# Optimization experiments

Hardware: AMD Instinct MI355X
Metric: run time of the kernel (lower is better)

## Reference

```python
import jax, jax.numpy as jnp
import numpy as np


def setup_inputs() -> dict:
    key = jax.random.key(0)
    ks = jax.random.split(key, 8)
    B, L, D, N, K = 4, 4096, 1024, 64, 4
    return {
        "x": jax.random.normal(ks[0], (B, L, D), dtype=jnp.float32),
        "conv_w": jax.random.normal(ks[1], (K, 1, D), dtype=jnp.float32) * 0.1,
        "conv_b": jnp.zeros((D,), dtype=jnp.float32),
        "Wp": jax.random.normal(ks[2], (D, 2 * N), dtype=jnp.float32) * (1.0 / np.sqrt(D)),
        "bp": jnp.zeros((2 * N,), dtype=jnp.float32),
        "Ws": jax.random.normal(ks[3], (D, N), dtype=jnp.float32) * (1.0 / np.sqrt(D)),
        "bs": jnp.zeros((N,), dtype=jnp.float32),
        "A_log": jax.random.normal(ks[4], (N,), dtype=jnp.float32) * 0.02,
        "dt_log": jax.random.normal(ks[5], (N,), dtype=jnp.float32) * 0.02,
        "Wo": jax.random.normal(ks[6], (N, D), dtype=jnp.float32) * (1.0 / np.sqrt(N)),
        "bo": jnp.zeros((D,), dtype=jnp.float32),
    }


def reference(x, conv_w, conv_b, Wp, bp, Ws, bs, A_log, dt_log, Wo, bo):
    B, L, D = x.shape
    K = conv_w.shape[0]
    N = Ws.shape[1]

    # causal depthwise conv: left-pad by K-1, sum K shifted slices (K is tiny)
    x_pad = jnp.pad(x, ((0, 0), (K - 1, 0), (0, 0)))
    conv = conv_b + sum(x_pad[:, k:k + L, :] * conv_w[k, 0] for k in range(K))

    proj = conv @ Wp + bp                     # [B, L, 2N]
    B_t = jax.nn.softplus(proj[..., :N])      # [B, L, N]
    C_t = jnp.tanh(proj[..., N:])             # [B, L, N]
    u = x @ Ws + bs                           # [B, L, N]

    A = -jax.nn.softplus(A_log)               # [N]
    dt = jax.nn.softplus(dt_log)              # [N]
    decay = 1.0 + dt * A                      # [N]

    def step(state, inputs):
        u_t, b_t, c_t = inputs                # each [B, N]
        state = decay * state + dt * b_t * u_t
        return state, c_t * state

    init = jnp.zeros((B, N), dtype=x.dtype)
    xs = tuple(jnp.swapaxes(a, 0, 1) for a in (u, B_t, C_t))  # time-major
    _, ys = jax.lax.scan(step, init, xs, unroll=4)            # [L, B, N]
    y = jnp.swapaxes(ys, 0, 1)                                # [B, L, N]
    return y @ Wo + bo                                        # [B, L, D]
```

## Files before the change

kernel.cpp:

```cpp
#include <hip/hip_runtime.h>

#define B_ 4
#define L_ 4096
#define D_ 1024
#define N_ 64

typedef _Float16 f16;
typedef __attribute__((ext_vector_type(8))) _Float16 half8;
typedef __attribute__((ext_vector_type(4))) float f32x4;

__device__ __forceinline__ float softplus_f(float x) {
    return fmaxf(x, 0.0f) + log1pf(__expf(-fabsf(x)));
}

__device__ __forceinline__ float tanh_f(float x) {
    float xc = fminf(fmaxf(x, -15.0f), 15.0f);
    float e = __expf(2.0f * xc);
    return (e - 1.0f) / (e + 1.0f);
}

__global__ __launch_bounds__(256) void k_prepw(
    const float* __restrict__ Wp, const float* __restrict__ Ws,
    const float* __restrict__ Wo, f16* __restrict__ WT, f16* __restrict__ WoT)
{
    int gid = blockIdx.x * 256 + threadIdx.x;
    if (gid < 24576) {
        int r = gid >> 7, kg = gid & 127;
        const float* src; int ncol, c;
        if (r < 128) { src = Wp; ncol = 128; c = r; }
        else         { src = Ws; ncol = 64;  c = r - 128; }
        f16 h[8];
        #pragma unroll
        for (int j = 0; j < 8; j++)
            h[j] = (f16)src[(size_t)(kg * 8 + j) * ncol + c];
        *(uint4*)&WT[(size_t)r * 1024 + kg * 8] = *(uint4*)h;
    } else {
        int g2 = gid - 24576;
        int d = g2 >> 3, ng = g2 & 7;
        f16 h[8];
        #pragma unroll
        for (int j = 0; j < 8; j++)
            h[j] = (f16)Wo[(size_t)(ng * 8 + j) * D_ + d];
        *(uint4*)&WoT[(size_t)d * 64 + ng * 8] = *(uint4*)h;
    }
}

__global__ __launch_bounds__(256) void k_frontend(
    const float* __restrict__ x, const float* __restrict__ conv_w,
    const float* __restrict__ conv_b, const f16* __restrict__ WT,
    const float* __restrict__ bp, const float* __restrict__ bs,
    const float* __restrict__ dt_log,
    f16* __restrict__ zT, f16* __restrict__ cT)
{
    __shared__ __align__(16) f16 xh[36 * 72];
    __shared__ float sE[3 * 32 * 68];

    const int tid = threadIdx.x;
    const int w = tid >> 6, lane = tid & 63;
    const int r = lane & 15, q = lane >> 4;
    const int T0 = blockIdx.x * 32;
    const int bb = T0 >> 12;
    const int l0 = T0 & (L_ - 1);
    const int cw0 = w * 48;

    f32x4 acc[3][2] = {};
    float4 rA[3];

    #define LDX(c0)                                                          \
        {                                                                    \
            _Pragma("unroll")                                                \
            for (int s = 0; s < 3; s++) {                                    \
                int idx = tid + 256 * s;                                     \
                float4 v = make_float4(0.f, 0.f, 0.f, 0.f);                  \
                if (idx < 576) {                                             \
                    int row = idx >> 4, g = idx & 15;                        \
                    int l = l0 + row - 4;                                    \
                    if (l >= 0)                                              \
                        v = *(const float4*)&x[((size_t)(bb * L_ + l)) * D_  \
                                               + (c0) + g * 4];              \
                }                                                            \
                rA[s] = v;                                                   \
            }                                                                \
        }

    LDX(0);
    for (int c = 0; c < 16; c++) {
        __syncthreads();
        #pragma unroll
        for (int s = 0; s < 3; s++) {
            int idx = tid + 256 * s;
            if (idx < 576) {
                int row = idx >> 4, g = idx & 15;
                f16 h[4] = {(f16)rA[s].x, (f16)rA[s].y, (f16)rA[s].z, (f16)rA[s].w};
                *(uint2*)&xh[row * 72 + g * 4] = *(uint2*)h;
            }
        }
        __syncthreads();
        if (c < 15) LDX((c + 1) * 64);

        const int k0 = c * 64;
        #pragma unroll
        for (int ks = 0; ks < 2; ks++) {
            const int kk = k0 + ks * 32 + q * 8;
            const int kl = ks * 32 + q * 8;

            half8 af[3];
            #pragma unroll
            for (int mf = 0; mf < 3; mf++)
                af[mf] = *(const half8*)&WT[(size_t)(cw0 + mf * 16 + r) * 1024 + kk];

            float cw3[8], cw2[8], cw1[8], cw0v[8], cbv[8];
            if (w < 3) {
                float4 a0 = *(const float4*)&conv_w[3 * D_ + kk];
                float4 a1 = *(const float4*)&conv_w[3 * D_ + kk + 4];
                float4 b0 = *(const float4*)&conv_w[2 * D_ + kk];
                float4 b1 = *(const float4*)&conv_w[2 * D_ + kk + 4];
                float4 c0v = *(const float4*)&conv_w[1 * D_ + kk];
                float4 c1v = *(const float4*)&conv_w[1 * D_ + kk + 4];
                float4 d0v = *(const float4*)&conv_w[0 * D_ + kk];
                float4 d1v = *(const float4*)&conv_w[0 * D_ + kk + 4];
                float4 e0 = *(const float4*)&conv_b[kk];
                float4 e1 = *(const float4*)&conv_b[kk + 4];
                cw3[0]=a0.x;cw3[1]=a0.y;cw3[2]=a0.z;cw3[3]=a0.w;cw3[4]=a1.x;cw3[5]=a1.y;cw3[6]=a1.z;cw3[7]=a1.w;
                cw2[0]=b0.x;cw2[1]=b0.y;cw2[2]=b0.z;cw2[3]=b0.w;cw2[4]=b1.x;cw2[5]=b1.y;cw2[6]=b1.z;cw2[7]=b1.w;
                cw1[0]=c0v.x;cw1[1]=c0v.y;cw1[2]=c0v.z;cw1[3]=c0v.w;cw1[4]=c1v.x;cw1[5]=c1v.y;cw1[6]=c1v.z;cw1[7]=c1v.w;
                cw0v[0]=d0v.x;cw0v[1]=d0v.y;cw0v[2]=d0v.z;cw0v[3]=d0v.w;cw0v[4]=d1v.x;cw0v[5]=d1v.y;cw0v[6]=d1v.z;cw0v[7]=d1v.w;
                cbv[0]=e0.x;cbv[1]=e0.y;cbv[2]=e0.z;cbv[3]=e0.w;cbv[4]=e1.x;cbv[5]=e1.y;cbv[6]=e1.z;cbv[7]=e1.w;
            }

            half8 braw[2], bcnv[2];
            #pragma unroll
            for (int nf = 0; nf < 2; nf++) {
                const int rb = nf * 16 + r + 4;
                half8 h0 = *(const half8*)&xh[rb * 72 + kl];
                braw[nf] = h0;
                if (w < 3) {
                    half8 h1 = *(const half8*)&xh[(rb - 1) * 72 + kl];
                    half8 h2 = *(const half8*)&xh[(rb - 2) * 72 + kl];
                    half8 h3 = *(const half8*)&xh[(rb - 3) * 72 + kl];
                    half8 hc;
                    #pragma unroll
                    for (int u = 0; u < 8; u++) {
                        float s0 = cbv[u];
                        s0 = fmaf(cw3[u], (float)h0[u], s0);
                        s0 = fmaf(cw2[u], (float)h1[u], s0);
                        s0 = fmaf(cw1[u], (float)h2[u], s0);
                        s0 = fmaf(cw0v[u], (float)h3[u], s0);
                        hc[u] = (f16)s0;
                    }
                    bcnv[nf] = hc;
                }
            }

            #pragma unroll
            for (int mf = 0; mf < 3; mf++) {
                const bool useConv = (cw0 + mf * 16) < 128;
                #pragma unroll
                for (int nf = 0; nf < 2; nf++)
                    acc[mf][nf] = __builtin_amdgcn_mfma_f32_16x16x32_f16(
                        af[mf], useConv ? bcnv[nf] : braw[nf], acc[mf][nf], 0, 0, 0);
            }
        }
    }

    float* sB = sE;
    float* sC = sE + 32 * 68;
    float* sU = sE + 2 * 32 * 68;
    __syncthreads();
    #pragma unroll
    for (int mf = 0; mf < 3; mf++) {
        const int cb4 = cw0 + mf * 16 + q * 4;
        const int seg = cb4 >> 6;
        const int cl = cb4 & 63;
        const float4 bb4 = (seg == 2) ? *(const float4*)&bs[cl]
                                      : *(const float4*)&bp[cb4];
        float* dst = (seg == 0) ? sB : (seg == 1 ? sC : sU);
        #pragma unroll
        for (int nf = 0; nf < 2; nf++) {
            const int t = nf * 16 + r;
            float v0 = acc[mf][nf][0] + bb4.x;
            float v1 = acc[mf][nf][1] + bb4.y;
            float v2 = acc[mf][nf][2] + bb4.z;
            float v3 = acc[mf][nf][3] + bb4.w;
            if (seg == 0) {
                v0 = softplus_f(v0); v1 = softplus_f(v1);
                v2 = softplus_f(v2); v3 = softplus_f(v3);
            } else if (seg == 1) {
                v0 = tanh_f(v0); v1 = tanh_f(v1);
                v2 = tanh_f(v2); v3 = tanh_f(v3);
            }
            float4 vv = {v0, v1, v2, v3};
            *(float4*)&dst[t * 68 + cl] = vv;
        }
    }
    __syncthreads();

    {
        const int n = tid >> 2, tg = tid & 3;
        const float dtv = softplus_f(dt_log[n]);
        f16 hz[8], hc[8];
        #pragma unroll
        for (int j = 0; j < 8; j++) {
            const int t = tg * 8 + j;
            hz[j] = (f16)(dtv * sB[t * 68 + n] * sU[t * 68 + n]);
            hc[j] = (f16)sC[t * 68 + n];
        }
        size_t o = ((size_t)(bb * N_ + n)) * L_ + l0 + tg * 8;
        *(uint4*)&zT[o] = *(uint4*)hz;
        *(uint4*)&cT[o] = *(uint4*)hc;
    }
    #undef LDX
}

__global__ __launch_bounds__(64) void k_scan(
    const f16* __restrict__ zT, const f16* __restrict__ cT,
    const float* __restrict__ A_log, const float* __restrict__ dt_log,
    f16* __restrict__ yH)
{
    __shared__ float zs[L_];
    __shared__ float cs[L_];
    const int bn = blockIdx.x;
    const int n = bn & (N_ - 1);
    const int lane = threadIdx.x;
    const f16* zp = zT + (size_t)bn * L_;
    const f16* cp = cT + (size_t)bn * L_;

    for (int it = 0; it < 8; it++) {
        int i = lane * 8 + it * 512;
        uint4 rz = *(const uint4*)(zp + i);
        uint4 rc = *(const uint4*)(cp + i);
        const f16* hz = (const f16*)&rz;
        const f16* hc = (const f16*)&rc;
        #pragma unroll
        for (int k = 0; k < 8; k++) {
            zs[i + k] = (float)hz[k];
            cs[i + k] = (float)hc[k];
        }
    }
    __syncthreads();

    float dtv = softplus_f(dt_log[n]);
    float Av = -softplus_f(A_log[n]);
    float dec = fmaf(dtv, Av, 1.0f);

    float s = 0.0f;
    const int base = lane * 64;
    #pragma unroll
    for (int j = 0; j < 64; j++) s = fmaf(dec, s, zs[base + j]);

    float d2 = dec * dec, d4 = d2 * d2, d8 = d4 * d4;
    float d16 = d8 * d8, d32 = d16 * d16, d64 = d32 * d32;

    float Ag = d64, Bg = s;
    #pragma unroll
    for (int off = 1; off < 64; off <<= 1) {
        float Ap = __shfl_up(Ag, off);
        float Bp = __shfl_up(Bg, off);
        if (lane >= off) { Bg = fmaf(Ag, Bp, Bg); Ag *= Ap; }
    }
    float carry = __shfl_up(Bg, 1);
    if (lane == 0) carry = 0.0f;

    float st = carry;
    #pragma unroll
    for (int j = 0; j < 64; j++) {
        st = fmaf(dec, st, zs[base + j]);
        zs[base + j] = cs[base + j] * st;
    }
    __syncthreads();
    f16* yp = yH + (size_t)bn * L_;
    for (int i = lane * 8; i < L_; i += 512) {
        f16 h[8];
        #pragma unroll
        for (int k = 0; k < 8; k++) h[k] = (f16)zs[i + k];
        *(uint4*)&yp[i] = *(uint4*)h;
    }
}

__global__ __launch_bounds__(256) void k_out(
    const f16* __restrict__ yH, const f16* __restrict__ WoT,
    const float* __restrict__ bo, float* __restrict__ out)
{
    __shared__ __align__(16) f16 ys[64 * 72];
    const int tid = threadIdx.x;
    const int w = tid >> 6, lane = tid & 63;
    const int r = lane & 15, q = lane >> 4;
    const int T0 = blockIdx.x * 64;
    const int bb = T0 >> 12, l0 = T0 & (L_ - 1);
    const int dw = blockIdx.y * 128 + w * 32;

    {
        const int n = tid & 63, tg = tid >> 6;
        #pragma unroll
        for (int h2 = 0; h2 < 2; h2++) {
            uint4 v = *(const uint4*)&yH[((size_t)(bb * N_ + n)) * L_ + l0 + tg * 16 + h2 * 8];
            const f16* hh = (const f16*)&v;
            #pragma unroll
            for (int j = 0; j < 8; j++)
                ys[(tg * 16 + h2 * 8 + j) * 72 + n] = hh[j];
        }
    }
    __syncthreads();

    f32x4 acc[2][4] = {};
    #pragma unroll
    for (int ks = 0; ks < 2; ks++) {
        const int kk = ks * 32 + q * 8;
        half8 af[2];
        #pragma unroll
        for (int mf = 0; mf < 2; mf++)
            af[mf] = *(const half8*)&WoT[(size_t)(dw + mf * 16 + r) * 64 + kk];
        #pragma unroll
        for (int nf = 0; nf < 4; nf++) {
            half8 bf = *(const half8*)&ys[(nf * 16 + r) * 72 + kk];
            #pragma unroll
            for (int mf = 0; mf < 2; mf++)
                acc[mf][nf] = __builtin_amdgcn_mfma_f32_16x16x32_f16(
                    af[mf], bf, acc[mf][nf], 0, 0, 0);
        }
    }

    #pragma unroll
    for (int mf = 0; mf < 2; mf++) {
        const int d = dw + mf * 16 + q * 4;
        const float4 bb4 = *(const float4*)&bo[d];
        #pragma unroll
        for (int nf = 0; nf < 4; nf++) {
            const int t = T0 + nf * 16 + r;
            float4 o = {acc[mf][nf][0] + bb4.x, acc[mf][nf][1] + bb4.y,
                        acc[mf][nf][2] + bb4.z, acc[mf][nf][3] + bb4.w};
            *(float4*)&out[(size_t)t * D_ + d] = o;
        }
    }
}

extern "C" void kernel_launch(void* const* d_in, const int* in_sizes, int n_in,
                              void* d_out, int out_size, void* d_ws, size_t ws_size,
                              hipStream_t stream) {
    const float* x      = (const float*)d_in[0];
    const float* conv_w = (const float*)d_in[1];
    const float* conv_b = (const float*)d_in[2];
    const float* Wp     = (const float*)d_in[3];
    const float* bp     = (const float*)d_in[4];
    const float* Ws     = (const float*)d_in[5];
    const float* bs     = (const float*)d_in[6];
    const float* A_log  = (const float*)d_in[7];
    const float* dt_log = (const float*)d_in[8];
    const float* Wo     = (const float*)d_in[9];
    const float* bo     = (const float*)d_in[10];
    float* out = (float*)d_out;

    char* wsp = (char*)d_ws;
    f16* WT  = (f16*)wsp;
    f16* WoT = (f16*)(wsp + 393216);
    f16* zT  = (f16*)(wsp + 524288);
    f16* cT  = (f16*)(wsp + 2621440);
    f16* yH  = (f16*)(wsp + 4718592);

    k_prepw<<<dim3(128), dim3(256), 0, stream>>>(Wp, Ws, Wo, WT, WoT);
    k_frontend<<<dim3(B_ * L_ / 32), dim3(256), 0, stream>>>(
        x, conv_w, conv_b, WT, bp, bs, dt_log, zT, cT);
    k_scan<<<dim3(B_ * N_), dim3(64), 0, stream>>>(zT, cT, A_log, dt_log, yH);
    k_out<<<dim3(B_ * L_ / 64, D_ / 128), dim3(256), 0, stream>>>(yH, WoT, bo, out);
}
```

Before: 198.7 us.

## Split frontend GEMM K across two wave groups and compute conv once into LDS

The frontend block grows from 256 to 512 threads. The two wave groups each take half of every 64-wide K chunk, and their partial accumulators are reduced through LDS before the activation step. The depthwise conv is now computed once per chunk into a shared LDS tile, using conv weights staged in LDS, instead of being recomputed redundantly by three waves from global memory. This adds an extra barrier per chunk and more LDS use, which could lower occupancy.

```diff
diff --git a/kernel.cpp b/kernel.cpp
--- a/kernel.cpp
+++ b/kernel.cpp
@@ -45,7 +45,7 @@
     }
 }
 
-__global__ __launch_bounds__(256) void k_frontend(
+__global__ __launch_bounds__(512) void k_frontend(
     const float* __restrict__ x, const float* __restrict__ conv_w,
     const float* __restrict__ conv_b, const f16* __restrict__ WT,
     const float* __restrict__ bp, const float* __restrict__ bs,
@@ -53,112 +53,118 @@
     f16* __restrict__ zT, f16* __restrict__ cT)
 {
     __shared__ __align__(16) f16 xh[36 * 72];
+    __shared__ __align__(16) f16 ch[32 * 72];
+    __shared__ __align__(16) float cwS[5 * 1024];
     __shared__ float sE[3 * 32 * 68];
 
     const int tid = threadIdx.x;
     const int w = tid >> 6, lane = tid & 63;
     const int r = lane & 15, q = lane >> 4;
+    const int wq = w & 3, wk = w >> 2;
     const int T0 = blockIdx.x * 32;
     const int bb = T0 >> 12;
     const int l0 = T0 & (L_ - 1);
-    const int cw0 = w * 48;
+    const int cw0 = wq * 48;
 
     f32x4 acc[3][2] = {};
-    float4 rA[3];
+    float4 rA, rB;
+
+    for (int i = tid; i < 1280; i += 512) {
+        float4 v = (i < 1024) ? ((const float4*)conv_w)[i]
+                              : ((const float4*)conv_b)[i - 1024];
+        ((float4*)cwS)[i] = v;
+    }
 
     #define LDX(c0)                                                          \
         {                                                                    \
-            _Pragma("unroll")                                                \
-            for (int s = 0; s < 3; s++) {                                    \
-                int idx = tid + 256 * s;                                     \
+            {                                                                \
+                int row = tid >> 4, g = tid & 15;                            \
+                int l = l0 + row - 4;                                        \
                 float4 v = make_float4(0.f, 0.f, 0.f, 0.f);                  \
-                if (idx < 576) {                                             \
-                    int row = idx >> 4, g = idx & 15;                        \
-                    int l = l0 + row - 4;                                    \
-                    if (l >= 0)                                              \
-                        v = *(const float4*)&x[((size_t)(bb * L_ + l)) * D_  \
-                                               + (c0) + g * 4];              \
-                }                                                            \
-                rA[s] = v;                                                   \
+                if (l >= 0)                                                  \
+                    v = *(const float4*)&x[((size_t)(bb * L_ + l)) * D_      \
+                                           + (c0) + g * 4];                  \
+                rA = v;                                                      \
+            }                                                                \
+            if (tid < 64) {                                                  \
+                int row = 32 + (tid >> 4), g = tid & 15;                     \
+                int l = l0 + row - 4;                                        \
+                rB = *(const float4*)&x[((size_t)(bb * L_ + l)) * D_         \
+                                        + (c0) + g * 4];                     \
             }                                                                \
         }
 
     LDX(0);
     for (int c = 0; c < 16; c++) {
         __syncthreads();
-        #pragma unroll
-        for (int s = 0; s < 3; s++) {
-            int idx = tid + 256 * s;
-            if (idx < 576) {
-                int row = idx >> 4, g = idx & 15;
-                f16 h[4] = {(f16)rA[s].x, (f16)rA[s].y, (f16)rA[s].z, (f16)rA[s].w};
-                *(uint2*)&xh[row * 72 + g * 4] = *(uint2*)h;
+        {
+            int row = tid >> 4, g = tid & 15;
+            f16 h[4] = {(f16)rA.x, (f16)rA.y, (f16)rA.z, (f16)rA.w};
+            *(uint2*)&xh[row * 72 + g * 4] = *(uint2*)h;
+            if (tid < 64) {
+                int row2 = 32 + (tid >> 4);
+                f16 h2[4] = {(f16)rB.x, (f16)rB.y, (f16)rB.z, (f16)rB.w};
+                *(uint2*)&xh[row2 * 72 + g * 4] = *(uint2*)h2;
             }
         }
         __syncthreads();
         if (c < 15) LDX((c + 1) * 64);
 
-        const int k0 = c * 64;
-        #pragma unroll
-        for (int ks = 0; ks < 2; ks++) {
-            const int kk = k0 + ks * 32 + q * 8;
-            const int kl = ks * 32 + q * 8;
-
-            half8 af[3];
-            #pragma unroll
-            for (int mf = 0; mf < 3; mf++)
-                af[mf] = *(const half8*)&WT[(size_t)(cw0 + mf * 16 + r) * 1024 + kk];
-
-            float cw3[8], cw2[8], cw1[8], cw0v[8], cbv[8];
-            if (w < 3) {
-                float4 a0 = *(const float4*)&conv_w[3 * D_ + kk];
-                float4 a1 = *(const float4*)&conv_w[3 * D_ + kk + 4];
-                float4 b0 = *(const float4*)&conv_w[2 * D_ + kk];
-                float4 b1 = *(const float4*)&conv_w[2 * D_ + kk + 4];
-                float4 c0v = *(const float4*)&conv_w[1 * D_ + kk];
-                float4 c1v = *(const float4*)&conv_w[1 * D_ + kk + 4];
-                float4 d0v = *(const float4*)&conv_w[0 * D_ + kk];
-                float4 d1v = *(const float4*)&conv_w[0 * D_ + kk + 4];
-                float4 e0 = *(const float4*)&conv_b[kk];
-                float4 e1 = *(const float4*)&conv_b[kk + 4];
-                cw3[0]=a0.x;cw3[1]=a0.y;cw3[2]=a0.z;cw3[3]=a0.w;cw3[4]=a1.x;cw3[5]=a1.y;cw3[6]=a1.z;cw3[7]=a1.w;
-                cw2[0]=b0.x;cw2[1]=b0.y;cw2[2]=b0.z;cw2[3]=b0.w;cw2[4]=b1.x;cw2[5]=b1.y;cw2[6]=b1.z;cw2[7]=b1.w;
-                cw1[0]=c0v.x;cw1[1]=c0v.y;cw1[2]=c0v.z;cw1[3]=c0v.w;cw1[4]=c1v.x;cw1[5]=c1v.y;cw1[6]=c1v.z;cw1[7]=c1v.w;
-                cw0v[0]=d0v.x;cw0v[1]=d0v.y;cw0v[2]=d0v.z;cw0v[3]=d0v.w;cw0v[4]=d1v.x;cw0v[5]=d1v.y;cw0v[6]=d1v.z;cw0v[7]=d1v.w;
-                cbv[0]=e0.x;cbv[1]=e0.y;cbv[2]=e0.z;cbv[3]=e0.w;cbv[4]=e1.x;cbv[5]=e1.y;cbv[6]=e1.z;cbv[7]=e1.w;
-            }
-
-            half8 braw[2], bcnv[2];
-            #pragma unroll
-            for (int nf = 0; nf < 2; nf++) {
-                const int rb = nf * 16 + r + 4;
-                half8 h0 = *(const half8*)&xh[rb * 72 + kl];
-                braw[nf] = h0;
-                if (w < 3) {
-                    half8 h1 = *(const half8*)&xh[(rb - 1) * 72 + kl];
-                    half8 h2 = *(const half8*)&xh[(rb - 2) * 72 + kl];
-                    half8 h3 = *(const half8*)&xh[(rb - 3) * 72 + kl];
-                    half8 hc;
-                    #pragma unroll
-                    for (int u = 0; u < 8; u++) {
-                        float s0 = cbv[u];
-                        s0 = fmaf(cw3[u], (float)h0[u], s0);
-                        s0 = fmaf(cw2[u], (float)h1[u], s0);
-                        s0 = fmaf(cw1[u], (float)h2[u], s0);
-                        s0 = fmaf(cw0v[u], (float)h3[u], s0);
-                        hc[u] = (f16)s0;
-                    }
-                    bcnv[nf] = hc;
-                }
-            }
-
+        const int kl = wk * 32 + q * 8;
+        const int kk = c * 64 + kl;
+        half8 af0 = *(const half8*)&WT[(size_t)(cw0 + r) * 1024 + kk];
+        half8 af1 = *(const half8*)&WT[(size_t)(cw0 + 16 + r) * 1024 + kk];
+        half8 af2 = *(const half8*)&WT[(size_t)(cw0 + 32 + r) * 1024 + kk];
+
+        {
+            const int row = tid >> 4;
+            const int d4 = (tid & 15) * 4;
+            const int dg = c * 64 + d4;
+            f32x4 w0 = *(const f32x4*)&cwS[dg];
+            f32x4 w1 = *(const f32x4*)&cwS[1024 + dg];
+            f32x4 w2 = *(const f32x4*)&cwS[2048 + dg];
+            f32x4 w3 = *(const f32x4*)&cwS[3072 + dg];
+            f32x4 cb = *(const f32x4*)&cwS[4096 + dg];
+            f16 x0[4], x1[4], x2[4], x3[4], ho[4];
+            *(uint2*)x0 = *(const uint2*)&xh[(row + 1) * 72 + d4];
+            *(uint2*)x1 = *(const uint2*)&xh[(row + 2) * 72 + d4];
+            *(uint2*)x2 = *(const uint2*)&xh[(row + 3) * 72 + d4];
+            *(uint2*)x3 = *(const uint2*)&xh[(row + 4) * 72 + d4];
+            #pragma unroll
+            for (int j = 0; j < 4; j++) {
+                float s = cb[j];
+                s = fmaf(w0[j], (float)x0[j], s);
+                s = fmaf(w1[j], (float)x1[j], s);
+                s = fmaf(w2[j], (float)x2[j], s);
+                s = fmaf(w3[j], (float)x3[j], s);
+                ho[j] = (f16)s;
+            }
+            *(uint2*)&ch[row * 72 + d4] = *(uint2*)ho;
+        }
+        __syncthreads();
+
+        {
+            half8 bc8[2] = {}, br8[2] = {};
+            const bool needC = (cw0 < 128);
+            const bool needR = (cw0 + 32 >= 128);
+            if (needC) {
+                #pragma unroll
+                for (int nf = 0; nf < 2; nf++)
+                    bc8[nf] = *(const half8*)&ch[(nf * 16 + r) * 72 + kl];
+            }
+            if (needR) {
+                #pragma unroll
+                for (int nf = 0; nf < 2; nf++)
+                    br8[nf] = *(const half8*)&xh[(nf * 16 + r + 4) * 72 + kl];
+            }
             #pragma unroll
             for (int mf = 0; mf < 3; mf++) {
                 const bool useConv = (cw0 + mf * 16) < 128;
+                half8 a8 = (mf == 0) ? af0 : ((mf == 1) ? af1 : af2);
                 #pragma unroll
                 for (int nf = 0; nf < 2; nf++)
                     acc[mf][nf] = __builtin_amdgcn_mfma_f32_16x16x32_f16(
-                        af[mf], useConv ? bcnv[nf] : braw[nf], acc[mf][nf], 0, 0, 0);
+                        a8, useConv ? bc8[nf] : br8[nf], acc[mf][nf], 0, 0, 0);
             }
         }
     }
@@ -166,48 +172,67 @@
     float* sB = sE;
     float* sC = sE + 32 * 68;
     float* sU = sE + 2 * 32 * 68;
-    __syncthreads();
-    #pragma unroll
-    for (int mf = 0; mf < 3; mf++) {
-        const int cb4 = cw0 + mf * 16 + q * 4;
-        const int seg = cb4 >> 6;
-        const int cl = cb4 & 63;
-        const float4 bb4 = (seg == 2) ? *(const float4*)&bs[cl]
-                                      : *(const float4*)&bp[cb4];
-        float* dst = (seg == 0) ? sB : (seg == 1 ? sC : sU);
-        #pragma unroll
-        for (int nf = 0; nf < 2; nf++) {
-            const int t = nf * 16 + r;
-            float v0 = acc[mf][nf][0] + bb4.x;
-            float v1 = acc[mf][nf][1] + bb4.y;
-            float v2 = acc[mf][nf][2] + bb4.z;
-            float v3 = acc[mf][nf][3] + bb4.w;
-            if (seg == 0) {
-                v0 = softplus_f(v0); v1 = softplus_f(v1);
-                v2 = softplus_f(v2); v3 = softplus_f(v3);
-            } else if (seg == 1) {
-                v0 = tanh_f(v0); v1 = tanh_f(v1);
-                v2 = tanh_f(v2); v3 = tanh_f(v3);
-            }
-            float4 vv = {v0, v1, v2, v3};
-            *(float4*)&dst[t * 68 + cl] = vv;
+    if (wk == 0) {
+        #pragma unroll
+        for (int mf = 0; mf < 3; mf++) {
+            const int cb4 = cw0 + mf * 16 + q * 4;
+            const int seg = cb4 >> 6;
+            const int cl = cb4 & 63;
+            float* dst = (seg == 0) ? sB : (seg == 1 ? sC : sU);
+            #pragma unroll
+            for (int nf = 0; nf < 2; nf++) {
+                const int t = nf * 16 + r;
+                float4 vv = {acc[mf][nf][0], acc[mf][nf][1],
+                             acc[mf][nf][2], acc[mf][nf][3]};
+                *(float4*)&dst[t * 68 + cl] = vv;
+            }
+        }
+    }
+    __syncthreads();
+    if (wk == 1) {
+        #pragma unroll
+        for (int mf = 0; mf < 3; mf++) {
+            const int cb4 = cw0 + mf * 16 + q * 4;
+            const int seg = cb4 >> 6;
+            const int cl = cb4 & 63;
+            const float4 bb4 = (seg == 2) ? *(const float4*)&bs[cl]
+                                          : *(const float4*)&bp[cb4];
+            float* dst = (seg == 0) ? sB : (seg == 1 ? sC : sU);
+            #pragma unroll
+            for (int nf = 0; nf < 2; nf++) {
+                const int t = nf * 16 + r;
+                float4 p = *(float4*)&dst[t * 68 + cl];
+                float v0 = acc[mf][nf][0] + p.x + bb4.x;
+                float v1 = acc[mf][nf][1] + p.y + bb4.y;
+                float v2 = acc[mf][nf][2] + p.z + bb4.z;
+                float v3 = acc[mf][nf][3] + p.w + bb4.w;
+                if (seg == 0) {
+                    v0 = softplus_f(v0); v1 = softplus_f(v1);
+                    v2 = softplus_f(v2); v3 = softplus_f(v3);
+                } else if (seg == 1) {
+                    v0 = tanh_f(v0); v1 = tanh_f(v1);
+                    v2 = tanh_f(v2); v3 = tanh_f(v3);
+                }
+                float4 vv = {v0, v1, v2, v3};
+                *(float4*)&dst[t * 68 + cl] = vv;
+            }
         }
     }
     __syncthreads();
 
     {
-        const int n = tid >> 2, tg = tid & 3;
+        const int n = tid >> 3, tg = tid & 7;
         const float dtv = softplus_f(dt_log[n]);
-        f16 hz[8], hc[8];
-        #pragma unroll
-        for (int j = 0; j < 8; j++) {
-            const int t = tg * 8 + j;
+        f16 hz[4], hc[4];
+        #pragma unroll
+        for (int j = 0; j < 4; j++) {
+            const int t = tg * 4 + j;
             hz[j] = (f16)(dtv * sB[t * 68 + n] * sU[t * 68 + n]);
             hc[j] = (f16)sC[t * 68 + n];
         }
-        size_t o = ((size_t)(bb * N_ + n)) * L_ + l0 + tg * 8;
-        *(uint4*)&zT[o] = *(uint4*)hz;
-        *(uint4*)&cT[o] = *(uint4*)hc;
+        size_t o = ((size_t)(bb * N_ + n)) * L_ + l0 + tg * 4;
+        *(uint2*)&zT[o] = *(uint2*)hz;
+        *(uint2*)&cT[o] = *(uint2*)hc;
     }
     #undef LDX
 }
@@ -358,7 +383,7 @@
     f16* yH  = (f16*)(wsp + 4718592);
 
     k_prepw<<<dim3(128), dim3(256), 0, stream>>>(Wp, Ws, Wo, WT, WoT);
-    k_frontend<<<dim3(B_ * L_ / 32), dim3(256), 0, stream>>>(
+    k_frontend<<<dim3(B_ * L_ / 32), dim3(512), 0, stream>>>(
         x, conv_w, conv_b, WT, bp, bs, dt_log, zT, cT);
     k_scan<<<dim3(B_ * N_), dim3(64), 0, stream>>>(zT, cT, A_log, dt_log, yH);
     k_out<<<dim3(B_ * L_ / 64, D_ / 128), dim3(256), 0, stream>>>(yH, WoT, bo, out);
```

Result: slower. 259.6 us (+30.7%).

## Fold depthwise conv weights into projection matrix and run conv via MFMA

Applied to the files above, without the earlier changes.

The causal depthwise convolution is folded algebraically into the projection: the prep kernel builds four per-tap weight matrices conv_w[k]*Wp plus an effective bias conv_b@Wp+bp. The frontend then accumulates four shifted-row MFMAs instead of computing the conv on vector ALUs and converting to fp16 per tile. This removes the per-element conv FMAs, the conv_w loads and the warp imbalance (only 3 of 4 waves did conv). In exchange the projection does four times the MFMA work and loads four times the weight fragments, and rounding now happens on the products rather than on the conv output.

```diff
diff --git a/kernel.cpp b/kernel.cpp
--- a/kernel.cpp
+++ b/kernel.cpp
@@ -20,35 +20,52 @@
 }
 
 __global__ __launch_bounds__(256) void k_prepw(
-    const float* __restrict__ Wp, const float* __restrict__ Ws,
-    const float* __restrict__ Wo, f16* __restrict__ WT, f16* __restrict__ WoT)
+    const float* __restrict__ conv_w, const float* __restrict__ conv_b,
+    const float* __restrict__ Wp, const float* __restrict__ bp,
+    const float* __restrict__ Ws, const float* __restrict__ Wo,
+    f16* __restrict__ WT2, f16* __restrict__ WoT, float* __restrict__ bpE)
 {
     int gid = blockIdx.x * 256 + threadIdx.x;
-    if (gid < 24576) {
-        int r = gid >> 7, kg = gid & 127;
-        const float* src; int ncol, c;
-        if (r < 128) { src = Wp; ncol = 128; c = r; }
-        else         { src = Ws; ncol = 64;  c = r - 128; }
+    if (gid < 73728) {
+        int row = gid >> 7, kg = gid & 127;
         f16 h[8];
-        #pragma unroll
-        for (int j = 0; j < 8; j++)
-            h[j] = (f16)src[(size_t)(kg * 8 + j) * ncol + c];
-        *(uint4*)&WT[(size_t)r * 1024 + kg * 8] = *(uint4*)h;
-    } else {
-        int g2 = gid - 24576;
+        if (row < 512) {
+            int k = row >> 7, cc = row & 127;
+            #pragma unroll
+            for (int j = 0; j < 8; j++) {
+                int d = kg * 8 + j;
+                h[j] = (f16)(conv_w[k * D_ + d] * Wp[(size_t)d * 128 + cc]);
+            }
+        } else {
+            int cc = row - 512;
+            #pragma unroll
+            for (int j = 0; j < 8; j++)
+                h[j] = (f16)Ws[(size_t)(kg * 8 + j) * 64 + cc];
+        }
+        *(uint4*)&WT2[(size_t)row * 1024 + kg * 8] = *(uint4*)h;
+    } else if (gid < 81920) {
+        int g2 = gid - 73728;
         int d = g2 >> 3, ng = g2 & 7;
         f16 h[8];
         #pragma unroll
         for (int j = 0; j < 8; j++)
             h[j] = (f16)Wo[(size_t)(ng * 8 + j) * D_ + d];
         *(uint4*)&WoT[(size_t)d * 64 + ng * 8] = *(uint4*)h;
+    } else {
+        int idx = gid - 81920;
+        int cc = idx >> 1, hh = idx & 1;
+        float s = 0.0f;
+        #pragma unroll 4
+        for (int d = hh * 512; d < hh * 512 + 512; d++)
+            s = fmaf(conv_b[d], Wp[(size_t)d * 128 + cc], s);
+        s += __shfl_xor(s, 1);
+        if (hh == 0) bpE[cc] = bp[cc] + s;
     }
 }
 
 __global__ __launch_bounds__(256) void k_frontend(
-    const float* __restrict__ x, const float* __restrict__ conv_w,
-    const float* __restrict__ conv_b, const f16* __restrict__ WT,
-    const float* __restrict__ bp, const float* __restrict__ bs,
+    const float* __restrict__ x, const f16* __restrict__ WT2,
+    const float* __restrict__ bpE, const float* __restrict__ bs,
     const float* __restrict__ dt_log,
     f16* __restrict__ zT, f16* __restrict__ cT)
 {
@@ -61,9 +78,11 @@
     const int T0 = blockIdx.x * 32;
     const int bb = T0 >> 12;
     const int l0 = T0 & (L_ - 1);
-    const int cw0 = w * 48;
-
-    f32x4 acc[3][2] = {};
+    const int cp0 = w * 32;
+    const int cu0 = w * 16;
+
+    f32x4 accp[2][2] = {};
+    f32x4 accu[2] = {};
     float4 rA[3];
 
     #define LDX(c0)                                                          \
@@ -101,64 +120,43 @@
         const int k0 = c * 64;
         #pragma unroll
         for (int ks = 0; ks < 2; ks++) {
-            const int kk = k0 + ks * 32 + q * 8;
             const int kl = ks * 32 + q * 8;
-
-            half8 af[3];
-            #pragma unroll
-            for (int mf = 0; mf < 3; mf++)
-                af[mf] = *(const half8*)&WT[(size_t)(cw0 + mf * 16 + r) * 1024 + kk];
-
-            float cw3[8], cw2[8], cw1[8], cw0v[8], cbv[8];
-            if (w < 3) {
-                float4 a0 = *(const float4*)&conv_w[3 * D_ + kk];
-                float4 a1 = *(const float4*)&conv_w[3 * D_ + kk + 4];
-                float4 b0 = *(const float4*)&conv_w[2 * D_ + kk];
-                float4 b1 = *(const float4*)&conv_w[2 * D_ + kk + 4];
-                float4 c0v = *(const float4*)&conv_w[1 * D_ + kk];
-                float4 c1v = *(const float4*)&conv_w[1 * D_ + kk + 4];
-                float4 d0v = *(const float4*)&conv_w[0 * D_ + kk];
-                float4 d1v = *(const float4*)&conv_w[0 * D_ + kk + 4];
-                float4 e0 = *(const float4*)&conv_b[kk];
-                float4 e1 = *(const float4*)&conv_b[kk + 4];
-                cw3[0]=a0.x;cw3[1]=a0.y;cw3[2]=a0.z;cw3[3]=a0.w;cw3[4]=a1.x;cw3[5]=a1.y;cw3[6]=a1.z;cw3[7]=a1.w;
-                cw2[0]=b0.x;cw2[1]=b0.y;cw2[2]=b0.z;cw2[3]=b0.w;cw2[4]=b1.x;cw2[5]=b1.y;cw2[6]=b1.z;cw2[7]=b1.w;
-                cw1[0]=c0v.x;cw1[1]=c0v.y;cw1[2]=c0v.z;cw1[3]=c0v.w;cw1[4]=c1v.x;cw1[5]=c1v.y;cw1[6]=c1v.z;cw1[7]=c1v.w;
-                cw0v[0]=d0v.x;cw0v[1]=d0v.y;cw0v[2]=d0v.z;cw0v[3]=d0v.w;cw0v[4]=d1v.x;cw0v[5]=d1v.y;cw0v[6]=d1v.z;cw0v[7]=d1v.w;
-                cbv[0]=e0.x;cbv[1]=e0.y;cbv[2]=e0.z;cbv[3]=e0.w;cbv[4]=e1.x;cbv[5]=e1.y;cbv[6]=e1.z;cbv[7]=e1.w;
-            }
-
-            half8 braw[2], bcnv[2];
+            const int kk = k0 + kl;
+
+            half8 ap[2][4];
+            #pragma unroll
+            for (int mf = 0; mf < 2; mf++)
+                #pragma unroll
+                for (int k = 0; k < 4; k++)
+                    ap[mf][k] = *(const half8*)&WT2[
+                        (size_t)(k * 128 + cp0 + mf * 16 + r) * 1024 + kk];
+            half8 au = *(const half8*)&WT2[(size_t)(512 + cu0 + r) * 1024 + kk];
+
             #pragma unroll
             for (int nf = 0; nf < 2; nf++) {
-                const int rb = nf * 16 + r + 4;
-                half8 h0 = *(const half8*)&xh[rb * 72 + kl];
-                braw[nf] = h0;
-                if (w < 3) {
-                    half8 h1 = *(const half8*)&xh[(rb - 1) * 72 + kl];
-                    half8 h2 = *(const half8*)&xh[(rb - 2) * 72 + kl];
-                    half8 h3 = *(const half8*)&xh[(rb - 3) * 72 + kl];
-                    half8 hc;
-                    #pragma unroll
-                    for (int u = 0; u < 8; u++) {
-                        float s0 = cbv[u];
-                        s0 = fmaf(cw3[u], (float)h0[u], s0);
-                        s0 = fmaf(cw2[u], (float)h1[u], s0);
-                        s0 = fmaf(cw1[u], (float)h2[u], s0);
-                        s0 = fmaf(cw0v[u], (float)h3[u], s0);
-                        hc[u] = (f16)s0;
-                    }
-                    bcnv[nf] = hc;
-                }
-            }
-
-            #pragma unroll
-            for (int mf = 0; mf < 3; mf++) {
-                const bool useConv = (cw0 + mf * 16) < 128;
-                #pragma unroll
-                for (int nf = 0; nf < 2; nf++)
-                    acc[mf][nf] = __builtin_amdgcn_mfma_f32_16x16x32_f16(
-                        af[mf], useConv ? bcnv[nf] : braw[nf], acc[mf][nf], 0, 0, 0);
+                const int rb = nf * 16 + r;
+                half8 b0 = *(const half8*)&xh[(rb + 1) * 72 + kl];
+                half8 b1 = *(const half8*)&xh[(rb + 2) * 72 + kl];
+                half8 b2 = *(const half8*)&xh[(rb + 3) * 72 + kl];
+                half8 b3 = *(const half8*)&xh[(rb + 4) * 72 + kl];
+                accp[0][nf] = __builtin_amdgcn_mfma_f32_16x16x32_f16(
+                    ap[0][0], b0, accp[0][nf], 0, 0, 0);
+                accp[1][nf] = __builtin_amdgcn_mfma_f32_16x16x32_f16(
+                    ap[1][0], b0, accp[1][nf], 0, 0, 0);
+                accp[0][nf] = __builtin_amdgcn_mfma_f32_16x16x32_f16(
+                    ap[0][1], b1, accp[0][nf], 0, 0, 0);
+                accp[1][nf] = __builtin_amdgcn_mfma_f32_16x16x32_f16(
+                    ap[1][1], b1, accp[1][nf], 0, 0, 0);
+                accp[0][nf] = __builtin_amdgcn_mfma_f32_16x16x32_f16(
+                    ap[0][2], b2, accp[0][nf], 0, 0, 0);
+                accp[1][nf] = __builtin_amdgcn_mfma_f32_16x16x32_f16(
+                    ap[1][2], b2, accp[1][nf], 0, 0, 0);
+                accp[0][nf] = __builtin_amdgcn_mfma_f32_16x16x32_f16(
+                    ap[0][3], b3, accp[0][nf], 0, 0, 0);
+                accp[1][nf] = __builtin_amdgcn_mfma_f32_16x16x32_f16(
+                    ap[1][3], b3, accp[1][nf], 0, 0, 0);
+                accu[nf] = __builtin_amdgcn_mfma_f32_16x16x32_f16(
+                    au, b3, accu[nf], 0, 0, 0);
             }
         }
     }
@@ -168,29 +166,39 @@
     float* sU = sE + 2 * 32 * 68;
     __syncthreads();
     #pragma unroll
-    for (int mf = 0; mf < 3; mf++) {
-        const int cb4 = cw0 + mf * 16 + q * 4;
+    for (int mf = 0; mf < 2; mf++) {
+        const int cb4 = cp0 + mf * 16 + q * 4;
         const int seg = cb4 >> 6;
         const int cl = cb4 & 63;
-        const float4 bb4 = (seg == 2) ? *(const float4*)&bs[cl]
-                                      : *(const float4*)&bp[cb4];
-        float* dst = (seg == 0) ? sB : (seg == 1 ? sC : sU);
+        const float4 bb4 = *(const float4*)&bpE[cb4];
+        float* dst = seg ? sC : sB;
         #pragma unroll
         for (int nf = 0; nf < 2; nf++) {
             const int t = nf * 16 + r;
-            float v0 = acc[mf][nf][0] + bb4.x;
-            float v1 = acc[mf][nf][1] + bb4.y;
-            float v2 = acc[mf][nf][2] + bb4.z;
-            float v3 = acc[mf][nf][3] + bb4.w;
+            float v0 = accp[mf][nf][0] + bb4.x;
+            float v1 = accp[mf][nf][1] + bb4.y;
+            float v2 = accp[mf][nf][2] + bb4.z;
+            float v3 = accp[mf][nf][3] + bb4.w;
             if (seg == 0) {
                 v0 = softplus_f(v0); v1 = softplus_f(v1);
                 v2 = softplus_f(v2); v3 = softplus_f(v3);
-            } else if (seg == 1) {
+            } else {
                 v0 = tanh_f(v0); v1 = tanh_f(v1);
                 v2 = tanh_f(v2); v3 = tanh_f(v3);
             }
             float4 vv = {v0, v1, v2, v3};
             *(float4*)&dst[t * 68 + cl] = vv;
+        }
+    }
+    {
+        const int cu = cu0 + q * 4;
+        const float4 bb4 = *(const float4*)&bs[cu];
+        #pragma unroll
+        for (int nf = 0; nf < 2; nf++) {
+            const int t = nf * 16 + r;
+            float4 vv = {accu[nf][0] + bb4.x, accu[nf][1] + bb4.y,
+                         accu[nf][2] + bb4.z, accu[nf][3] + bb4.w};
+            *(float4*)&sU[t * 68 + cu] = vv;
         }
     }
     __syncthreads();
@@ -351,15 +359,17 @@
     float* out = (float*)d_out;
 
     char* wsp = (char*)d_ws;
-    f16* WT  = (f16*)wsp;
-    f16* WoT = (f16*)(wsp + 393216);
-    f16* zT  = (f16*)(wsp + 524288);
-    f16* cT  = (f16*)(wsp + 2621440);
-    f16* yH  = (f16*)(wsp + 4718592);
-
-    k_prepw<<<dim3(128), dim3(256), 0, stream>>>(Wp, Ws, Wo, WT, WoT);
+    f16* WT2   = (f16*)wsp;
+    f16* WoT   = (f16*)(wsp + 1179648);
+    float* bpE = (float*)(wsp + 1310720);
+    f16* zT    = (f16*)(wsp + 1311744);
+    f16* cT    = (f16*)(wsp + 3408896);
+    f16* yH    = (f16*)(wsp + 5506048);
+
+    k_prepw<<<dim3(321), dim3(256), 0, stream>>>(
+        conv_w, conv_b, Wp, bp, Ws, Wo, WT2, WoT, bpE);
     k_frontend<<<dim3(B_ * L_ / 32), dim3(256), 0, stream>>>(
-        x, conv_w, conv_b, WT, bp, bs, dt_log, zT, cT);
+        x, WT2, bpE, bs, dt_log, zT, cT);
     k_scan<<<dim3(B_ * N_), dim3(64), 0, stream>>>(zT, cT, A_log, dt_log, yH);
     k_out<<<dim3(B_ * L_ / 64, D_ / 128), dim3(256), 0, stream>>>(yH, WoT, bo, out);
 }
```

Result: slower. 241.7 us (+21.6%).
